# Kernel optimization log

Hardware: AMD Instinct MI355X
Metric: run time of the kernel (lower is better)

Reference implementation:

```python
import jax, jax.numpy as jnp
import numpy as np

NEG_SLOPE = 0.01  # torch leaky_relu default

def _lrelu(x):
    return jax.nn.leaky_relu(x, NEG_SLOPE)

def _l2norm(x, axis):
    # torch F.normalize(p=2, eps=1e-12)
    n = jnp.linalg.norm(x, axis=axis, keepdims=True)
    return x / jnp.maximum(n, 1e-12)

def setup_inputs() -> dict:
    key = jax.random.key(0)
    ks = jax.random.split(key, 12)
    Nda, Nq, C, Din, Dout = 10000, 64, 1024, 128, 256
    target_adj = (jax.random.uniform(ks[0], (Nda, Nda)) < 0.002).astype(jnp.float32)
    query_adj = (jax.random.uniform(ks[1], (Nq, Nq)) < 0.2).astype(jnp.float32)
    node_features_da = jax.random.normal(ks[2], (Nda, Din), dtype=jnp.float32)
    node_features_q = jax.random.normal(ks[3], (Nq, Din), dtype=jnp.float32)
    candidate_set = jax.random.randint(ks[4], (C,), 0, Nda)
    candidate_adj = (jax.random.uniform(ks[5], (C, C)) < 0.01).astype(jnp.float32)
    s_in = 1.0 / np.sqrt(Din).astype(np.float32)
    s_out = 1.0 / np.sqrt(Dout).astype(np.float32)
    W1_da = jax.random.normal(ks[6], (Din, Dout), dtype=jnp.float32) * s_in
    W1_q = jax.random.normal(ks[7], (Din, Dout), dtype=jnp.float32) * s_in
    W2_da = jax.random.normal(ks[8], (Dout, Dout), dtype=jnp.float32) * s_out
    W2_q = jax.random.normal(ks[9], (Dout, Dout), dtype=jnp.float32) * s_out
    threshold = jnp.float32(0.2)
    return {"target_adj": target_adj, "node_features_da": node_features_da,
            "query_adj": query_adj, "node_features_q": node_features_q,
            "candidate_set": candidate_set, "candidate_adj": candidate_adj,
            "threshold": threshold, "W1_da": W1_da, "W1_q": W1_q,
            "W2_da": W2_da, "W2_q": W2_q}

def _cross_cosine(q, da, candidate_set):
    # cosine similarity between each query node and each candidate target node: [Nq, C]
    return _l2norm(q, 1) @ _l2norm(da[candidate_set], 1).T

def reference(target_adj, node_features_da, query_adj, node_features_q,
              candidate_set, candidate_adj, threshold, W1_da, W1_q, W2_da, W2_q):
    # layer 1: GCN propagation on both graphs (gcn(adj,x) = adj @ x @ W)
    da1 = _lrelu(target_adj @ (node_features_da @ W1_da))   # [Nda, D]
    q1 = _lrelu(query_adj @ (node_features_q @ W1_q))       # [Nq, D]
    c1 = _cross_cosine(q1, da1, candidate_set)               # [Nq, C]
    pre_da1 = da1[candidate_set]                             # [C, D]
    # NOTE: da1[candidate_set].data = ... mutates a temporary in torch -> no-op on da1
    att_da1 = _lrelu(da1)                                    # dropout in eval = identity
    h1_q = c1 @ pre_da1                                      # [Nq, D]
    att_q1 = _lrelu(q1 + _l2norm(h1_q, 0))
    # layer 2
    da2 = _lrelu(target_adj @ (att_da1 @ W2_da))
    q2 = _lrelu(query_adj @ (att_q1 @ W2_q))
    c2 = _cross_cosine(q2, da2, candidate_set)
    pre_da2 = da2[candidate_set]
    att_da2 = _lrelu(da2)                                    # in-place update is again a no-op
    h2_q = c2 @ pre_da2
    att_q2 = _lrelu(q2 + _l2norm(h2_q, 0))
    # graph-level matching score per target node
    emb = jnp.mean(att_q2, axis=0, keepdims=True)            # [1, D]
    num = att_da2 @ emb[0]                                   # [Nda]
    den = jnp.maximum(jnp.linalg.norm(att_da2, axis=1) * jnp.linalg.norm(emb), 1e-8)
    end = (num / den)[None, :]                               # [1, Nda]
    # threshold selection expressed with a mask (jit-safe, same math: excluded
    # rows/cols are zero and do not affect L2 norms, sums, or the trace)
    m = (end[0] > threshold).astype(att_da2.dtype)           # [Nda]
    F_ = att_da2 * m[:, None]
    re_adj = F_ @ F_.T                                       # [Nda, Nda]
    nor_re = _l2norm(re_adj, 1) * target_adj                 # elementwise with original adj
    cnt = jnp.sum(m)
    total = jnp.sum(nor_re)
    tr = jnp.trace(nor_re)
    has = cnt > 0
    pre_avg_degree = jnp.where(has, total / jnp.maximum(cnt, 1.0), 0.0)
    pre_avg_nodes = jnp.where(has, tr, 0.0)
    pre_density = jnp.where(has, 2.0 * total / (tr * (tr - 1.0) + 1e-4), 0.0)
    return (end, att_da2, att_q2, pre_avg_degree, pre_density, pre_avg_nodes)
```

## Files before the change

### kernel.cpp

```cpp
#include <hip/hip_runtime.h>

constexpr int NDA = 10000;
constexpr int NQ  = 64;
constexpr int CND = 1024;
constexpr int DIN = 128;
constexpr int D   = 256;
constexpr int CAP = 96;

#define LRELU(x) ((x) >= 0.f ? (x) : 0.01f * (x))

__device__ __forceinline__ float wave_red64(float v) {
#pragma unroll
    for (int o = 32; o; o >>= 1) v += __shfl_down(v, o);
    return v;
}

__global__ __launch_bounds__(256) void build_csr(const float* __restrict__ adj,
                                                 int* __restrict__ cols,
                                                 int* __restrict__ rowcnt) {
    int row = blockIdx.x;
    __shared__ int scnt;
    if (threadIdx.x == 0) scnt = 0;
    __syncthreads();
    const float4* rp = (const float4*)(adj + (size_t)row * NDA);
    for (int i = threadIdx.x; i < NDA / 4; i += 256) {
        float4 v = rp[i];
        if (v.x != 0.f) { int s = atomicAdd(&scnt, 1); if (s < CAP) cols[row * CAP + s] = 4 * i; }
        if (v.y != 0.f) { int s = atomicAdd(&scnt, 1); if (s < CAP) cols[row * CAP + s] = 4 * i + 1; }
        if (v.z != 0.f) { int s = atomicAdd(&scnt, 1); if (s < CAP) cols[row * CAP + s] = 4 * i + 2; }
        if (v.w != 0.f) { int s = atomicAdd(&scnt, 1); if (s < CAP) cols[row * CAP + s] = 4 * i + 3; }
    }
    __syncthreads();
    if (threadIdx.x == 0) rowcnt[row] = min(scnt, CAP);
}

template <bool RELU_A, bool RELU_C>
__global__ __launch_bounds__(256) void gemm64(const float* __restrict__ A,
                                              const float* __restrict__ B,
                                              float* __restrict__ C,
                                              int M, int N, int K) {
    __shared__ float As[16][68];
    __shared__ float Bs[16][68];
    const int bm = blockIdx.x * 64;
    const int bn = blockIdx.y * 64;
    const int tid = threadIdx.x;
    const int tx = tid & 15, ty = tid >> 4;
    float acc[4][4] = {};
    for (int k0 = 0; k0 < K; k0 += 16) {
        {
            int m = tid >> 2;
            int k4 = (tid & 3) * 4;
            float4 v = make_float4(0.f, 0.f, 0.f, 0.f);
            if (bm + m < M) v = *(const float4*)(A + (size_t)(bm + m) * K + k0 + k4);
            if (RELU_A) { v.x = LRELU(v.x); v.y = LRELU(v.y); v.z = LRELU(v.z); v.w = LRELU(v.w); }
            As[k4 + 0][m] = v.x; As[k4 + 1][m] = v.y; As[k4 + 2][m] = v.z; As[k4 + 3][m] = v.w;
        }
        {
            int kk = tid >> 4;
            int n4 = (tid & 15) * 4;
            float4 v = *(const float4*)(B + (size_t)(k0 + kk) * N + bn + n4);
            Bs[kk][n4 + 0] = v.x; Bs[kk][n4 + 1] = v.y; Bs[kk][n4 + 2] = v.z; Bs[kk][n4 + 3] = v.w;
        }
        __syncthreads();
#pragma unroll
        for (int kk = 0; kk < 16; kk++) {
            float av[4], bv[4];
#pragma unroll
            for (int i = 0; i < 4; i++) av[i] = As[kk][ty * 4 + i];
#pragma unroll
            for (int j = 0; j < 4; j++) bv[j] = Bs[kk][tx * 4 + j];
#pragma unroll
            for (int i = 0; i < 4; i++)
#pragma unroll
                for (int j = 0; j < 4; j++) acc[i][j] += av[i] * bv[j];
        }
        __syncthreads();
    }
#pragma unroll
    for (int i = 0; i < 4; i++) {
        int r = bm + ty * 4 + i;
        if (r < M) {
            float4 v;
            v.x = acc[i][0]; v.y = acc[i][1]; v.z = acc[i][2]; v.w = acc[i][3];
            if (RELU_C) { v.x = LRELU(v.x); v.y = LRELU(v.y); v.z = LRELU(v.z); v.w = LRELU(v.w); }
            *(float4*)(C + (size_t)r * N + bn + tx * 4) = v;
        }
    }
}

__global__ __launch_bounds__(256) void spmm_csr(const int* __restrict__ cols,
                                                const int* __restrict__ rowcnt,
                                                const float* __restrict__ X,
                                                float* __restrict__ out1,
                                                float* __restrict__ out2) {
    int row = blockIdx.x;
    int d = threadIdx.x;
    int cnt = rowcnt[row];
    __shared__ int sc[CAP];
    if (d < cnt) sc[d] = cols[row * CAP + d];
    __syncthreads();
    float a0 = 0.f, a1 = 0.f, a2 = 0.f, a3 = 0.f;
    int k = 0;
    for (; k + 4 <= cnt; k += 4) {
        a0 += X[(size_t)sc[k + 0] * D + d];
        a1 += X[(size_t)sc[k + 1] * D + d];
        a2 += X[(size_t)sc[k + 2] * D + d];
        a3 += X[(size_t)sc[k + 3] * D + d];
    }
    for (; k < cnt; k++) a0 += X[(size_t)sc[k] * D + d];
    float v = LRELU(a0 + a1 + a2 + a3);
    out1[(size_t)row * D + d] = v;
    if (out2) out2[(size_t)row * D + d] = LRELU(v);
}

__global__ __launch_bounds__(256) void rownorms_kernel(const float* __restrict__ da,
                                                       const int* __restrict__ cand,
                                                       float* __restrict__ rnc,
                                                       const float* __restrict__ q,
                                                       float* __restrict__ rnq) {
    int b = blockIdx.x;
    const float* src;
    float* dst;
    if (b < CND) { src = da + (size_t)cand[b] * D; dst = rnc + b; }
    else         { src = q + (size_t)(b - CND) * D; dst = rnq + (b - CND); }
    float v = src[threadIdx.x];
    float p = wave_red64(v * v);
    __shared__ float red[4];
    int w = threadIdx.x >> 6, lane = threadIdx.x & 63;
    if (lane == 0) red[w] = p;
    __syncthreads();
    if (threadIdx.x == 0) *dst = sqrtf(red[0] + red[1] + red[2] + red[3]);
}

__global__ __launch_bounds__(256) void cosmat_kernel(const float* __restrict__ q,
                                                     const float* __restrict__ rnq,
                                                     const float* __restrict__ da,
                                                     const int* __restrict__ cand,
                                                     const float* __restrict__ rnc,
                                                     float* __restrict__ cm) {
    __shared__ float qs[D];
    int r = blockIdx.x;
    int cc = blockIdx.y * 256 + threadIdx.x;
    qs[threadIdx.x] = q[r * D + threadIdx.x];
    __syncthreads();
    int row = cand[cc];
    const float4* ap = (const float4*)(da + (size_t)row * D);
    float dot = 0.f;
#pragma unroll 8
    for (int k = 0; k < D / 4; k++) {
        float4 v = ap[k];
        dot += qs[4 * k] * v.x + qs[4 * k + 1] * v.y + qs[4 * k + 2] * v.z + qs[4 * k + 3] * v.w;
    }
    float denom = fmaxf(rnq[r], 1e-12f) * fmaxf(rnc[cc], 1e-12f);
    cm[r * CND + cc] = dot / denom;
}

__global__ __launch_bounds__(256) void hq_kernel(const float* __restrict__ cm,
                                                 const float* __restrict__ da,
                                                 const int* __restrict__ cand,
                                                 float* __restrict__ h) {
    __shared__ float swt[CND];
    __shared__ int sci[CND];
    int r = blockIdx.x, d = threadIdx.x;
    for (int s = 0; s < CND / 256; s++) {
        swt[s * 256 + d] = cm[r * CND + s * 256 + d];
        sci[s * 256 + d] = cand[s * 256 + d];
    }
    __syncthreads();
    float a0 = 0.f, a1 = 0.f, a2 = 0.f, a3 = 0.f, a4 = 0.f, a5 = 0.f, a6 = 0.f, a7 = 0.f;
    for (int c = 0; c < CND; c += 8) {
        a0 += swt[c + 0] * da[(size_t)sci[c + 0] * D + d];
        a1 += swt[c + 1] * da[(size_t)sci[c + 1] * D + d];
        a2 += swt[c + 2] * da[(size_t)sci[c + 2] * D + d];
        a3 += swt[c + 3] * da[(size_t)sci[c + 3] * D + d];
        a4 += swt[c + 4] * da[(size_t)sci[c + 4] * D + d];
        a5 += swt[c + 5] * da[(size_t)sci[c + 5] * D + d];
        a6 += swt[c + 6] * da[(size_t)sci[c + 6] * D + d];
        a7 += swt[c + 7] * da[(size_t)sci[c + 7] * D + d];
    }
    h[r * D + d] = ((a0 + a1) + (a2 + a3)) + ((a4 + a5) + (a6 + a7));
}

__global__ __launch_bounds__(256) void attq_kernel(const float* __restrict__ q,
                                                   const float* __restrict__ h,
                                                   float* __restrict__ attq,
                                                   float* __restrict__ emb) {
    int d = threadIdx.x;
    float hv[NQ];
    float ss = 0.f;
#pragma unroll
    for (int r = 0; r < NQ; r++) {
        hv[r] = h[r * D + d];
        ss += hv[r] * hv[r];
    }
    float inv = 1.f / fmaxf(sqrtf(ss), 1e-12f);
    float es = 0.f;
#pragma unroll
    for (int r = 0; r < NQ; r++) {
        float v = q[r * D + d] + hv[r] * inv;
        v = LRELU(v);
        attq[r * D + d] = v;
        es += v;
    }
    if (emb) {
        float e = es * (1.f / (float)NQ);
        emb[d] = e;
        float p = wave_red64(e * e);
        __shared__ float red[4];
        int w = d >> 6, lane = d & 63;
        if (lane == 0) red[w] = p;
        __syncthreads();
        if (d == 0) emb[D] = sqrtf(red[0] + red[1] + red[2] + red[3]);
    }
}

__global__ __launch_bounds__(256) void end_kernel(const float* __restrict__ A,
                                                  const float* __restrict__ emb,
                                                  const float* __restrict__ thr_p,
                                                  float* __restrict__ endv,
                                                  float* __restrict__ m,
                                                  float* __restrict__ cnt) {
    __shared__ float se[D];
    __shared__ float scnt;
    int d = threadIdx.x;
    se[d] = emb[d];
    if (d == 0) scnt = 0.f;
    __syncthreads();
    float embn = emb[D];
    float thr = *thr_p;
    int w = d >> 6, lane = d & 63;
    int row = blockIdx.x * 4 + w;
    const float* ar = A + (size_t)row * D;
    float num = 0.f, sq = 0.f;
#pragma unroll
    for (int s = 0; s < 4; s++) {
        float v = ar[lane + 64 * s];
        num += v * se[lane + 64 * s];
        sq += v * v;
    }
#pragma unroll
    for (int o = 32; o; o >>= 1) { num += __shfl_down(num, o); sq += __shfl_down(sq, o); }
    if (lane == 0) {
        float den = fmaxf(sqrtf(sq) * embn, 1e-8f);
        float e = num / den;
        endv[row] = e;
        float mv = e > thr ? 1.f : 0.f;
        m[row] = mv;
        if (mv != 0.f) atomicAdd(&scnt, 1.f);
    }
    __syncthreads();
    if (d == 0 && scnt != 0.f) atomicAdd(cnt, scnt);
}

constexpr int GCHUNK = 400;
__global__ __launch_bounds__(256) void G_kernel(const float* __restrict__ A,
                                                const float* __restrict__ m,
                                                float* __restrict__ G) {
    __shared__ float SA[8][64], SB[8][64];
    int ti = blockIdx.x >> 2, tj = blockIdx.x & 3;
    int base = blockIdx.y * GCHUNK;
    int tid = threadIdx.x;
    int tx = tid & 15, ty = tid >> 4;
    float acc[4][4] = {};
    for (int g0 = 0; g0 < GCHUNK; g0 += 8) {
        for (int l = tid; l < 512; l += 256) {
            int rr = l >> 6, c = l & 63;
            int r = base + g0 + rr;
            float mv = m[r];
            SA[rr][c] = A[(size_t)r * D + ti * 64 + c] * mv;
            SB[rr][c] = A[(size_t)r * D + tj * 64 + c];
        }
        __syncthreads();
#pragma unroll
        for (int rr = 0; rr < 8; rr++) {
            float av[4], bv[4];
#pragma unroll
            for (int i = 0; i < 4; i++) av[i] = SA[rr][ty * 4 + i];
#pragma unroll
            for (int j = 0; j < 4; j++) bv[j] = SB[rr][tx * 4 + j];
#pragma unroll
            for (int i = 0; i < 4; i++)
#pragma unroll
                for (int j = 0; j < 4; j++) acc[i][j] += av[i] * bv[j];
        }
        __syncthreads();
    }
#pragma unroll
    for (int i = 0; i < 4; i++)
#pragma unroll
        for (int j = 0; j < 4; j++)
            atomicAdd(&G[(ti * 64 + ty * 4 + i) * D + tj * 64 + tx * 4 + j], acc[i][j]);
}

__global__ __launch_bounds__(256) void final_kernel(const int* __restrict__ cols,
                                                    const int* __restrict__ rowcnt,
                                                    const float* __restrict__ m,
                                                    const float* __restrict__ A,
                                                    const float* __restrict__ H,
                                                    double* __restrict__ total,
                                                    double* __restrict__ tr) {
    int i = blockIdx.x;
    if (m[i] == 0.f) return;
    __shared__ float sa[D];
    __shared__ int sc[CAP];
    __shared__ float red[4], red2[4];
    __shared__ float sdenom;
    int d = threadIdx.x;
    float av = A[(size_t)i * D + d];
    sa[d] = av;
    int cnt = rowcnt[i];
    if (d < cnt) sc[d] = cols[i * CAP + d];
    float p = wave_red64(av * H[(size_t)i * D + d]);
    int w = d >> 6, lane = d & 63;
    if (lane == 0) red[w] = p;
    __syncthreads();
    if (d == 0) sdenom = fmaxf(sqrtf(red[0] + red[1] + red[2] + red[3]), 1e-12f);
    __syncthreads();
    float accs = 0.f, acct = 0.f;
    for (int k = w; k < cnt; k += 4) {
        int j = sc[k];
        if (m[j] != 0.f) {
            const float* aj = A + (size_t)j * D;
            float t = sa[lane] * aj[lane] + sa[lane + 64] * aj[lane + 64]
                    + sa[lane + 128] * aj[lane + 128] + sa[lane + 192] * aj[lane + 192];
            t = wave_red64(t);
            if (lane == 0) { accs += t; if (j == i) acct += t; }
        }
    }
    if (lane == 0) { red[w] = accs; red2[w] = acct; }
    __syncthreads();
    if (d == 0) {
        float s = red[0] + red[1] + red[2] + red[3];
        float t2 = red2[0] + red2[1] + red2[2] + red2[3];
        double inv = 1.0 / (double)sdenom;
        if (s != 0.f) atomicAdd(total, (double)s * inv);
        if (t2 != 0.f) atomicAdd(tr, (double)t2 * inv);
    }
}

__global__ void scalars_kernel(const float* __restrict__ cnt,
                               const double* __restrict__ total,
                               const double* __restrict__ tr,
                               float* __restrict__ out) {
    float c = *cnt;
    float T = (float)*total;
    float R = (float)*tr;
    bool has = c > 0.f;
    out[0] = has ? (T / fmaxf(c, 1.f)) : 0.f;
    out[1] = has ? (2.f * T / (R * (R - 1.f) + 1e-4f)) : 0.f;
    out[2] = has ? R : 0.f;
}

extern "C" void kernel_launch(void* const* d_in, const int* in_sizes, int n_in,
                              void* d_out, int out_size, void* d_ws, size_t ws_size,
                              hipStream_t stream) {
    (void)in_sizes; (void)n_in; (void)out_size; (void)ws_size;
    const float* adj  = (const float*)d_in[0];
    const float* Fda  = (const float*)d_in[1];
    const float* Qadj = (const float*)d_in[2];
    const float* Fq   = (const float*)d_in[3];
    const int*   cand = (const int*)d_in[4];
    const float* thr  = (const float*)d_in[6];
    const float* W1da = (const float*)d_in[7];
    const float* W1q  = (const float*)d_in[8];
    const float* W2da = (const float*)d_in[9];
    const float* W2q  = (const float*)d_in[10];

    float* out = (float*)d_out;
    float* o_end    = out;
    float* o_attda2 = out + NDA;
    float* o_attq2  = out + NDA + (size_t)NDA * D;
    float* o_sc     = o_attq2 + NQ * D;

    char* w = (char*)d_ws;
    size_t off = 0;
    auto alloc = [&](size_t b) { size_t r = off; off += (b + 255) & ~(size_t)255; return r; };
    float* bufA = (float*)(w + alloc((size_t)NDA * D * 4));
    float* bufB = (float*)(w + alloc((size_t)NDA * D * 4));
    float* bufC = (float*)(w + alloc((size_t)NDA * D * 4));
    int* colsb   = (int*)(w + alloc((size_t)NDA * CAP * 4));
    int* rowcntb = (int*)(w + alloc((size_t)NDA * 4));
    float* mbuf  = (float*)(w + alloc((size_t)NDA * 4));
    char* zbase = w + alloc(262144 + 256);
    float* Gb    = (float*)zbase;
    float* cntb  = (float*)(zbase + 262144);
    double* totb = (double*)(zbase + 262144 + 8);
    double* trb  = (double*)(zbase + 262144 + 16);
    float* xq   = (float*)(w + alloc((size_t)NQ * D * 4));
    float* q1b  = (float*)(w + alloc((size_t)NQ * D * 4));
    float* aq1  = (float*)(w + alloc((size_t)NQ * D * 4));
    float* q2b  = (float*)(w + alloc((size_t)NQ * D * 4));
    float* hb   = (float*)(w + alloc((size_t)NQ * D * 4));
    float* cm   = (float*)(w + alloc((size_t)NQ * CND * 4));
    float* rnc  = (float*)(w + alloc((size_t)CND * 4));
    float* rnq  = (float*)(w + alloc((size_t)NQ * 4));
    float* embb = (float*)(w + alloc((size_t)(D + 1) * 4));

    hipMemsetAsync(zbase, 0, 262144 + 256, stream);

    const dim3 gBig((NDA + 63) / 64, D / 64);
    const dim3 gSmall(1, D / 64);

    gemm64<false, false><<<gBig, 256, 0, stream>>>(Fda, W1da, bufA, NDA, D, DIN);
    build_csr<<<NDA, 256, 0, stream>>>(adj, colsb, rowcntb);
    gemm64<false, false><<<gSmall, 256, 0, stream>>>(Fq, W1q, xq, NQ, D, DIN);
    gemm64<false, true><<<gSmall, 256, 0, stream>>>(Qadj, xq, q1b, NQ, D, NQ);
    spmm_csr<<<NDA, 256, 0, stream>>>(colsb, rowcntb, bufA, bufB, (float*)nullptr);
    rownorms_kernel<<<CND + NQ, 256, 0, stream>>>(bufB, cand, rnc, q1b, rnq);
    cosmat_kernel<<<dim3(NQ, CND / 256), 256, 0, stream>>>(q1b, rnq, bufB, cand, rnc, cm);
    hq_kernel<<<NQ, 256, 0, stream>>>(cm, bufB, cand, hb);
    attq_kernel<<<1, 256, 0, stream>>>(q1b, hb, aq1, (float*)nullptr);
    gemm64<true, false><<<gBig, 256, 0, stream>>>(bufB, W2da, bufA, NDA, D, D);
    gemm64<false, false><<<gSmall, 256, 0, stream>>>(aq1, W2q, xq, NQ, D, D);
    gemm64<false, true><<<gSmall, 256, 0, stream>>>(Qadj, xq, q2b, NQ, D, NQ);
    spmm_csr<<<NDA, 256, 0, stream>>>(colsb, rowcntb, bufA, bufC, o_attda2);
    rownorms_kernel<<<CND + NQ, 256, 0, stream>>>(bufC, cand, rnc, q2b, rnq);
    cosmat_kernel<<<dim3(NQ, CND / 256), 256, 0, stream>>>(q2b, rnq, bufC, cand, rnc, cm);
    hq_kernel<<<NQ, 256, 0, stream>>>(cm, bufC, cand, hb);
    attq_kernel<<<1, 256, 0, stream>>>(q2b, hb, o_attq2, embb);
    end_kernel<<<NDA / 4, 256, 0, stream>>>(o_attda2, embb, thr, o_end, mbuf, cntb);
    G_kernel<<<dim3(16, NDA / GCHUNK), 256, 0, stream>>>(o_attda2, mbuf, Gb);
    gemm64<false, false><<<gBig, 256, 0, stream>>>(o_attda2, Gb, bufB, NDA, D, D);
    final_kernel<<<NDA, 256, 0, stream>>>(colsb, rowcntb, mbuf, o_attda2, bufB, totb, trb);
    scalars_kernel<<<1, 1, 0, stream>>>(cntb, totb, trb, o_sc);
}
```

Before: 1.028 ms.

## Vectorize SpMM gather and factor final row sum as dot with neighbor sum

The sparse gather in spmm_csr now has each wave handle a strided subset of neighbors with float4 loads, and the four per-wave partial rows are combined through shared memory. final_kernel first compacts the masked neighbor list with a shared atomic counter. It then sums those neighbor rows and takes a single dot product with row i, replacing one dot product plus wave reduction per neighbor. The diagonal term is computed separately as a self dot product. This trades many serialized per-neighbor reductions for vector gathers, at the cost of more shared memory and changed floating-point summation order.

```diff
diff --git a/kernel.cpp b/kernel.cpp
--- a/kernel.cpp
+++ b/kernel.cpp
@@ -94,23 +94,35 @@
                                                 float* __restrict__ out1,
                                                 float* __restrict__ out2) {
     int row = blockIdx.x;
-    int d = threadIdx.x;
+    int t = threadIdx.x;
+    int w = t >> 6, lane = t & 63;
     int cnt = rowcnt[row];
     __shared__ int sc[CAP];
-    if (d < cnt) sc[d] = cols[row * CAP + d];
-    __syncthreads();
-    float a0 = 0.f, a1 = 0.f, a2 = 0.f, a3 = 0.f;
-    int k = 0;
-    for (; k + 4 <= cnt; k += 4) {
-        a0 += X[(size_t)sc[k + 0] * D + d];
-        a1 += X[(size_t)sc[k + 1] * D + d];
-        a2 += X[(size_t)sc[k + 2] * D + d];
-        a3 += X[(size_t)sc[k + 3] * D + d];
-    }
-    for (; k < cnt; k++) a0 += X[(size_t)sc[k] * D + d];
-    float v = LRELU(a0 + a1 + a2 + a3);
-    out1[(size_t)row * D + d] = v;
-    if (out2) out2[(size_t)row * D + d] = LRELU(v);
+    __shared__ float part[4][256];
+    if (t < cnt) sc[t] = cols[row * CAP + t];
+    __syncthreads();
+    float4 acc = make_float4(0.f, 0.f, 0.f, 0.f);
+    int k = w;
+    for (; k + 12 < cnt; k += 16) {
+        float4 v0 = ((const float4*)(X + (size_t)sc[k]      * D))[lane];
+        float4 v1 = ((const float4*)(X + (size_t)sc[k + 4]  * D))[lane];
+        float4 v2 = ((const float4*)(X + (size_t)sc[k + 8]  * D))[lane];
+        float4 v3 = ((const float4*)(X + (size_t)sc[k + 12] * D))[lane];
+        acc.x += (v0.x + v1.x) + (v2.x + v3.x);
+        acc.y += (v0.y + v1.y) + (v2.y + v3.y);
+        acc.z += (v0.z + v1.z) + (v2.z + v3.z);
+        acc.w += (v0.w + v1.w) + (v2.w + v3.w);
+    }
+    for (; k < cnt; k += 4) {
+        float4 v0 = ((const float4*)(X + (size_t)sc[k] * D))[lane];
+        acc.x += v0.x; acc.y += v0.y; acc.z += v0.z; acc.w += v0.w;
+    }
+    *(float4*)&part[w][lane * 4] = acc;
+    __syncthreads();
+    float s = part[0][t] + part[1][t] + part[2][t] + part[3][t];
+    float v = LRELU(s);
+    out1[(size_t)row * D + t] = v;
+    if (out2) out2[(size_t)row * D + t] = LRELU(v);
 }
 
 __global__ __launch_bounds__(256) void rownorms_kernel(const float* __restrict__ da,
@@ -301,40 +313,63 @@
                                                     double* __restrict__ tr) {
     int i = blockIdx.x;
     if (m[i] == 0.f) return;
-    __shared__ float sa[D];
     __shared__ int sc[CAP];
-    __shared__ float red[4], red2[4];
-    __shared__ float sdenom;
-    int d = threadIdx.x;
-    float av = A[(size_t)i * D + d];
-    sa[d] = av;
+    __shared__ float part[4][256];
+    __shared__ int sn, sdiag;
+    __shared__ float r1[4], r2[4], r3[4];
+    int t = threadIdx.x;
+    int w = t >> 6, lane = t & 63;
     int cnt = rowcnt[i];
-    if (d < cnt) sc[d] = cols[i * CAP + d];
-    float p = wave_red64(av * H[(size_t)i * D + d]);
-    int w = d >> 6, lane = d & 63;
-    if (lane == 0) red[w] = p;
-    __syncthreads();
-    if (d == 0) sdenom = fmaxf(sqrtf(red[0] + red[1] + red[2] + red[3]), 1e-12f);
-    __syncthreads();
-    float accs = 0.f, acct = 0.f;
-    for (int k = w; k < cnt; k += 4) {
-        int j = sc[k];
+    if (t == 0) { sn = 0; sdiag = 0; }
+    __syncthreads();
+    if (t < cnt) {
+        int j = cols[i * CAP + t];
         if (m[j] != 0.f) {
-            const float* aj = A + (size_t)j * D;
-            float t = sa[lane] * aj[lane] + sa[lane + 64] * aj[lane + 64]
-                    + sa[lane + 128] * aj[lane + 128] + sa[lane + 192] * aj[lane + 192];
-            t = wave_red64(t);
-            if (lane == 0) { accs += t; if (j == i) acct += t; }
-        }
-    }
-    if (lane == 0) { red[w] = accs; red2[w] = acct; }
-    __syncthreads();
-    if (d == 0) {
-        float s = red[0] + red[1] + red[2] + red[3];
-        float t2 = red2[0] + red2[1] + red2[2] + red2[3];
-        double inv = 1.0 / (double)sdenom;
-        if (s != 0.f) atomicAdd(total, (double)s * inv);
-        if (t2 != 0.f) atomicAdd(tr, (double)t2 * inv);
+            int s = atomicAdd(&sn, 1);
+            sc[s] = j;
+            if (j == i) sdiag = 1;
+        }
+    }
+    __syncthreads();
+    int n = sn;
+    float4 acc = make_float4(0.f, 0.f, 0.f, 0.f);
+    int k = w;
+    for (; k + 12 < n; k += 16) {
+        float4 v0 = ((const float4*)(A + (size_t)sc[k]      * D))[lane];
+        float4 v1 = ((const float4*)(A + (size_t)sc[k + 4]  * D))[lane];
+        float4 v2 = ((const float4*)(A + (size_t)sc[k + 8]  * D))[lane];
+        float4 v3 = ((const float4*)(A + (size_t)sc[k + 12] * D))[lane];
+        acc.x += (v0.x + v1.x) + (v2.x + v3.x);
+        acc.y += (v0.y + v1.y) + (v2.y + v3.y);
+        acc.z += (v0.z + v1.z) + (v2.z + v3.z);
+        acc.w += (v0.w + v1.w) + (v2.w + v3.w);
+    }
+    for (; k < n; k += 4) {
+        float4 v0 = ((const float4*)(A + (size_t)sc[k] * D))[lane];
+        acc.x += v0.x; acc.y += v0.y; acc.z += v0.z; acc.w += v0.w;
+    }
+    *(float4*)&part[w][lane * 4] = acc;
+    __syncthreads();
+    float av = A[(size_t)i * D + t];
+    float hv = H[(size_t)i * D + t];
+    float sd = part[0][t] + part[1][t] + part[2][t] + part[3][t];
+    float p1 = av * sd, p2 = av * hv, p3 = av * av;
+#pragma unroll
+    for (int o = 32; o; o >>= 1) {
+        p1 += __shfl_down(p1, o);
+        p2 += __shfl_down(p2, o);
+        p3 += __shfl_down(p3, o);
+    }
+    if (lane == 0) { r1[w] = p1; r2[w] = p2; r3[w] = p3; }
+    __syncthreads();
+    if (t == 0) {
+        float num  = r1[0] + r1[1] + r1[2] + r1[3];
+        float den2 = r2[0] + r2[1] + r2[2] + r2[3];
+        float self = r3[0] + r3[1] + r3[2] + r3[3];
+        float denom = fmaxf(sqrtf(den2), 1e-12f);
+        double inv = 1.0 / (double)denom;
+        if (num != 0.f) atomicAdd(total, (double)num * inv);
+        if (sdiag) atomicAdd(tr, (double)self * inv);
     }
 }
 
```

New measurement: 1.029 ms. Within noise of the previous version (+0.1%).
